# Optimization experiments

Measured on AMD Instinct MI355X. Metric: run time of the kernel, lower is better.

## Reference

```python
import math
import jax, jax.numpy as jnp
import numpy as np

CHANNELS = 512
OUT_CHANNELS = 512
N_HEADS = 8
K_CHANNELS = CHANNELS // N_HEADS
WINDOW = 4


def _get_relative_embeddings(emb, length):
    # emb: [1, 2*WINDOW+1, d] -> [1, 2*length-1, d]
    max_rel = 2 * WINDOW + 1
    pad_length = max(0, length - (WINDOW + 1))
    start = max(0, WINDOW + 1 - length)
    end = max_rel + 2 * length - 1
    if pad_length > 0:
        emb = jnp.pad(emb, ((0, 0), (pad_length, pad_length), (0, 0)))
    return emb[:, start:end]


def _rel_to_abs(x):
    # x: [b, h, l, 2l-1] -> [b, h, l, l] via skewing trick
    b, h, l, _ = x.shape
    x = jnp.pad(x, ((0, 0), (0, 0), (0, 0), (0, 1)))
    x_flat = x.reshape(b, h, l * 2 * l)
    x_flat = jnp.pad(x_flat, ((0, 0), (0, 0), (0, l - 1)))
    return x_flat.reshape(b, h, l + 1, 2 * l - 1)[..., :l, l - 1:]


def _abs_to_rel(x):
    # x: [b, h, l, l] -> [b, h, l, 2l-1]
    b, h, l, _ = x.shape
    x = jnp.pad(x, ((0, 0), (0, 0), (0, 0), (0, l - 1)))
    x_flat = x.reshape(b, h, -1)
    x_flat = jnp.pad(x_flat, ((0, 0), (0, 0), (l, 0)))
    return x_flat.reshape(b, h, l, 2 * l)[..., 1:]


def setup_inputs() -> dict:
    key = jax.random.key(0)
    ks = jax.random.split(key, 12)
    B, T = 4, 1024
    w_std = 1.0 / math.sqrt(CHANNELS)
    rel_std = K_CHANNELS ** (-0.5)
    return {
        'x': jax.random.normal(ks[0], (B, T, CHANNELS), jnp.float32),
        'c': jax.random.normal(ks[1], (B, T, CHANNELS), jnp.float32),
        'Wq': jax.random.normal(ks[2], (CHANNELS, CHANNELS), jnp.float32) * w_std,
        'bq': jnp.zeros((CHANNELS,), jnp.float32),
        'Wk': jax.random.normal(ks[3], (CHANNELS, CHANNELS), jnp.float32) * w_std,
        'bk': jnp.zeros((CHANNELS,), jnp.float32),
        'Wv': jax.random.normal(ks[4], (CHANNELS, CHANNELS), jnp.float32) * w_std,
        'bv': jnp.zeros((CHANNELS,), jnp.float32),
        'Wo': jax.random.normal(ks[5], (CHANNELS, OUT_CHANNELS), jnp.float32) * w_std,
        'bo': jnp.zeros((OUT_CHANNELS,), jnp.float32),
        'emb_rel_k': jax.random.normal(ks[6], (1, 2 * WINDOW + 1, K_CHANNELS), jnp.float32) * rel_std,
        'emb_rel_v': jax.random.normal(ks[7], (1, 2 * WINDOW + 1, K_CHANNELS), jnp.float32) * rel_std,
    }


def reference(x, c, Wq, bq, Wk, bk, Wv, bv, Wo, bo, emb_rel_k, emb_rel_v):
    b, t_t, _ = x.shape
    t_s = c.shape[1]
    # 1x1 convs == pointwise dense projections
    q = x @ Wq + bq
    k = c @ Wk + bk
    v = c @ Wv + bv
    q = q.reshape(b, t_t, N_HEADS, K_CHANNELS).transpose(0, 2, 1, 3)
    k = k.reshape(b, t_s, N_HEADS, K_CHANNELS).transpose(0, 2, 1, 3)
    v = v.reshape(b, t_s, N_HEADS, K_CHANNELS).transpose(0, 2, 1, 3)
    q_scaled = q / math.sqrt(K_CHANNELS)
    scores = jnp.einsum('bhtd,bhsd->bhts', q_scaled, k)
    # relative position bias via skewing trick (heads_share=True -> rel emb head dim 1)
    rel_k = _get_relative_embeddings(emb_rel_k, t_s)[0]  # [2*t_s-1, d]
    rel_logits = jnp.einsum('bhtd,md->bhtm', q_scaled, rel_k)
    scores = scores + _rel_to_abs(rel_logits)
    p_attn = jax.nn.softmax(scores, axis=-1)
    out = jnp.einsum('bhts,bhsd->bhtd', p_attn, v)
    rel_w = _abs_to_rel(p_attn)  # [b, h, t, 2t-1]
    rel_v = _get_relative_embeddings(emb_rel_v, t_s)[0]  # [2*t_s-1, d]
    out = out + jnp.einsum('bhtm,md->bhtd', rel_w, rel_v)
    out = out.transpose(0, 2, 1, 3).reshape(b, t_t, CHANNELS)
    return out @ Wo + bo
```

## Files before the change

kernel.cpp:

```cpp
#include <hip/hip_runtime.h>
#include <hip/hip_bf16.h>

#define B_ 4
#define T_ 1024
#define C_ 512
#define H_ 8

typedef __attribute__((ext_vector_type(8))) short short8;
typedef __attribute__((ext_vector_type(4))) float floatx4;

__device__ __forceinline__ unsigned short f2bs(float f) {
    __hip_bfloat16 h = __float2bfloat16(f);
    return *(unsigned short*)&h;
}
__device__ __forceinline__ float bs2f(unsigned short u) {
    __hip_bfloat16 h;
    *(unsigned short*)&h = u;
    return __bfloat162float(h);
}

__device__ __forceinline__ void gload_lds16(const void* g, void* l) {
    __builtin_amdgcn_global_load_lds(
        (const __attribute__((address_space(1))) unsigned int*)g,
        (__attribute__((address_space(3))) unsigned int*)l, 16, 0, 0);
}

__global__ __launch_bounds__(256) void prep(
    const float* __restrict__ Wq, const float* __restrict__ Wk,
    const float* __restrict__ Wv, const float* __restrict__ Wo,
    const float* __restrict__ x, const float* __restrict__ cc,
    unsigned short* __restrict__ WT,
    unsigned short* __restrict__ Xb, unsigned short* __restrict__ Cb)
{
    __shared__ unsigned short tileT[32][33];
    const int r = blockIdx.x, tid = threadIdx.x;
    if (r < 1024) {
        const int w = r >> 8, tile = r & 255;
        const int k0 = (tile >> 4) * 32, n0 = (tile & 15) * 32;
        const float* W = (w == 0) ? Wq : (w == 1) ? Wk : (w == 2) ? Wv : Wo;
        unsigned short* out = WT + (size_t)w * 512 * 512;
        const int kk = tid >> 3, ns = (tid & 7) * 4;
        const float4 v = *(const float4*)&W[(size_t)(k0 + kk) * 512 + n0 + ns];
        tileT[ns + 0][kk] = f2bs(v.x);
        tileT[ns + 1][kk] = f2bs(v.y);
        tileT[ns + 2][kk] = f2bs(v.z);
        tileT[ns + 3][kk] = f2bs(v.w);
        __syncthreads();
        const int nn = tid >> 3, ks = (tid & 7) * 4;
        ushort4 o;
        o.x = tileT[nn][ks + 0]; o.y = tileT[nn][ks + 1];
        o.z = tileT[nn][ks + 2]; o.w = tileT[nn][ks + 3];
        *(ushort4*)&out[(size_t)(n0 + nn) * 512 + k0 + ks] = o;
    } else {
        const int bi = r - 1024;
        const bool isx = bi < 1024;
        const float* src = isx ? x : cc;
        unsigned short* dst = isx ? Xb : Cb;
        const int gid = ((bi & 1023) * 256 + tid) * 8;
        const float4 v0 = *(const float4*)&src[gid];
        const float4 v1 = *(const float4*)&src[gid + 4];
        ushort4 a, b;
        a.x = f2bs(v0.x); a.y = f2bs(v0.y); a.z = f2bs(v0.z); a.w = f2bs(v0.w);
        b.x = f2bs(v1.x); b.y = f2bs(v1.y); b.z = f2bs(v1.z); b.w = f2bs(v1.w);
        *(ushort4*)&dst[gid] = a;
        *(ushort4*)&dst[gid + 4] = b;
    }
}

__global__ __launch_bounds__(256) void qkv_mfma(
    const unsigned short* __restrict__ Xb, const unsigned short* __restrict__ Cb,
    const unsigned short* __restrict__ WT,
    const float* __restrict__ bq, const float* __restrict__ bk,
    const float* __restrict__ bv,
    unsigned short* __restrict__ Qc, unsigned short* __restrict__ Kc,
    unsigned short* __restrict__ Vtg)
{
    const int z = blockIdx.z;
    const unsigned short* Ab = (z == 0) ? Xb : Cb;
    const unsigned short* Bt = WT + (size_t)z * 262144;
    const float* bias = (z == 0) ? bq : (z == 1) ? bk : bv;
    const float scale = (z == 0) ? 0.18033688011112042f  : 1.0f;

    __shared__ __align__(16) unsigned short sA[3 * 128 * 32];
    __shared__ __align__(16) unsigned short sB[3 * 128 * 32];

    const int tid = threadIdx.x;
    const int wave = tid >> 6, lane = tid & 63;
    const int m0 = blockIdx.y * 128, n0 = blockIdx.x * 128;
    const int mrow = lane & 15, quad = lane >> 4, kgrp = quad * 8;
    const int mhalf = (wave & 1) * 64, noff = (wave >> 1) * 64;
    const int lrow = lane >> 2, lseg = (lane & 3) * 16;

    floatx4 acc[4][4];
    #pragma unroll
    for (int i = 0; i < 4; i++)
        #pragma unroll
        for (int j = 0; j < 4; j++)
            acc[i][j] = (floatx4){0.f, 0.f, 0.f, 0.f};

    auto stage = [&](int k0, int bufi) {
        #pragma unroll
        for (int j = 0; j < 2; j++) {
            const int rr = wave * 32 + j * 16 + lrow;
            gload_lds16((const char*)Ab + ((size_t)(m0 + rr) * 512 + k0) * 2 + lseg,
                        &sA[(size_t)(bufi * 128 + wave * 32 + j * 16) * 32]);
            gload_lds16((const char*)Bt + ((size_t)(n0 + rr) * 512 + k0) * 2 + lseg,
                        &sB[(size_t)(bufi * 128 + wave * 32 + j * 16) * 32]);
        }
    };

    stage(0, 0);
    stage(32, 1);
    for (int ck = 0; ck < 16; ck++) {
        const int buf = ck % 3;
        if (ck < 15) asm volatile("s_waitcnt vmcnt(4)" ::: "memory");
        else         asm volatile("s_waitcnt vmcnt(0)" ::: "memory");
        __builtin_amdgcn_s_barrier();
        __builtin_amdgcn_sched_barrier(0);
        if (ck < 14) stage((ck + 2) * 32, (ck + 2) % 3);
        const unsigned short* sAb = sA + (size_t)buf * 128 * 32;
        const unsigned short* sBb = sB + (size_t)buf * 128 * 32;
        short8 af[4], bfv[4];
        #pragma unroll
        for (int i = 0; i < 4; i++)
            af[i] = *(const short8*)&sAb[(size_t)(mhalf + i * 16 + mrow) * 32 + kgrp];
        #pragma unroll
        for (int i = 0; i < 4; i++)
            bfv[i] = *(const short8*)&sBb[(size_t)(noff + i * 16 + mrow) * 32 + kgrp];
        #pragma unroll
        for (int mt = 0; mt < 4; mt++)
            #pragma unroll
            for (int nt = 0; nt < 4; nt++)
                acc[mt][nt] = __builtin_amdgcn_mfma_f32_16x16x32_bf16(
                    af[mt], bfv[nt], acc[mt][nt], 0, 0, 0);
    }

    const int rowq = quad * 4;
    if (z < 2) {
        unsigned short* Y = (z == 0) ? Qc : Kc;
        #pragma unroll
        for (int nt = 0; nt < 4; nt++) {
            const int n = n0 + noff + nt * 16 + mrow;
            const float bv_ = bias[n];
            const int h = n >> 6, d = n & 63;
            #pragma unroll
            for (int mt = 0; mt < 4; mt++)
                #pragma unroll
                for (int r = 0; r < 4; r++) {
                    const int m = m0 + mhalf + mt * 16 + rowq + r;
                    const int bb = m >> 10, t = m & 1023;
                    Y[(((size_t)bb * H_ + h) * 1024 + t) * 64 + d] =
                        f2bs((acc[mt][nt][r] + bv_) * scale);
                }
        }
    } else {
        #pragma unroll
        for (int nt = 0; nt < 4; nt++) {
            const int n = n0 + noff + nt * 16 + mrow;
            const float bv_ = bias[n];
            const int h = n >> 6, d = n & 63;
            #pragma unroll
            for (int mt = 0; mt < 4; mt++) {
                const int m = m0 + mhalf + mt * 16 + rowq;
                const int bb = m >> 10, t = m & 1023;
                ushort4 o4;
                o4.x = f2bs(acc[mt][nt][0] + bv_);
                o4.y = f2bs(acc[mt][nt][1] + bv_);
                o4.z = f2bs(acc[mt][nt][2] + bv_);
                o4.w = f2bs(acc[mt][nt][3] + bv_);
                *(ushort4*)&Vtg[(((size_t)bb * H_ + h) * 64 + d) * 1024 + t] = o4;
            }
        }
    }
}

__global__ __launch_bounds__(256) void out_mfma(
    const unsigned short* __restrict__ AOb, const unsigned short* __restrict__ WoT,
    const float* __restrict__ bias, float* __restrict__ out)
{
    __shared__ __align__(16) unsigned short sA[3 * 128 * 32];
    __shared__ __align__(16) unsigned short sB[3 * 64 * 32];

    const int tid = threadIdx.x;
    const int wave = tid >> 6, lane = tid & 63;
    const int m0 = blockIdx.y * 128, n0 = blockIdx.x * 64;
    const int mrow = lane & 15, quad = lane >> 4, kgrp = quad * 8;
    const int mhalf = (wave & 1) * 64, noff = (wave >> 1) * 32;
    const int lrow = lane >> 2, lseg = (lane & 3) * 16;

    floatx4 acc[4][2];
    #pragma unroll
    for (int i = 0; i < 4; i++)
        #pragma unroll
        for (int j = 0; j < 2; j++)
            acc[i][j] = (floatx4){0.f, 0.f, 0.f, 0.f};

    auto stage = [&](int k0, int bufi) {
        #pragma unroll
        for (int j = 0; j < 2; j++) {
            const int rA = wave * 32 + j * 16 + lrow;
            gload_lds16((const char*)AOb + ((size_t)(m0 + rA) * 512 + k0) * 2 + lseg,
                        &sA[(size_t)(bufi * 128 + wave * 32 + j * 16) * 32]);
        }
        const int rB = wave * 16 + lrow;
        gload_lds16((const char*)WoT + ((size_t)(n0 + rB) * 512 + k0) * 2 + lseg,
                    &sB[(size_t)(bufi * 64 + wave * 16) * 32]);
    };

    stage(0, 0);
    stage(32, 1);
    for (int ck = 0; ck < 16; ck++) {
        const int buf = ck % 3;
        if (ck < 15) asm volatile("s_waitcnt vmcnt(3)" ::: "memory");
        else         asm volatile("s_waitcnt vmcnt(0)" ::: "memory");
        __builtin_amdgcn_s_barrier();
        __builtin_amdgcn_sched_barrier(0);
        if (ck < 14) stage((ck + 2) * 32, (ck + 2) % 3);
        const unsigned short* sAb = sA + (size_t)buf * 128 * 32;
        const unsigned short* sBb = sB + (size_t)buf * 64 * 32;
        short8 af[4], bfv[2];
        #pragma unroll
        for (int i = 0; i < 4; i++)
            af[i] = *(const short8*)&sAb[(size_t)(mhalf + i * 16 + mrow) * 32 + kgrp];
        #pragma unroll
        for (int i = 0; i < 2; i++)
            bfv[i] = *(const short8*)&sBb[(size_t)(noff + i * 16 + mrow) * 32 + kgrp];
        #pragma unroll
        for (int mt = 0; mt < 4; mt++)
            #pragma unroll
            for (int nt = 0; nt < 2; nt++)
                acc[mt][nt] = __builtin_amdgcn_mfma_f32_16x16x32_bf16(
                    af[mt], bfv[nt], acc[mt][nt], 0, 0, 0);
    }

    const int rowq = quad * 4;
    #pragma unroll
    for (int nt = 0; nt < 2; nt++) {
        const int n = n0 + noff + nt * 16 + mrow;
        const float bv_ = bias[n];
        #pragma unroll
        for (int mt = 0; mt < 4; mt++)
            #pragma unroll
            for (int r = 0; r < 4; r++) {
                const int m = m0 + mhalf + mt * 16 + rowq + r;
                out[(size_t)m * 512 + n] = acc[mt][nt][r] + bv_;
            }
    }
}

__device__ __forceinline__ void attn_stage(
    const unsigned short* __restrict__ Kc, const unsigned short* __restrict__ Vtg,
    size_t qkbase, size_t vtbase, int s0, int wave, int ldrow, int gseg,
    unsigned short* KLb, unsigned short* VtLb)
{
    #pragma unroll
    for (int j = 0; j < 2; j++) {
        const int br = wave * 16 + j * 8;
        gload_lds16((const char*)Kc + (qkbase + (size_t)(s0 + br + ldrow) * 64) * 2 + gseg * 16,
                    &KLb[br * 64]);
        gload_lds16((const char*)Vtg + (vtbase + (size_t)(br + ldrow) * 1024 + s0) * 2 + gseg * 16,
                    &VtLb[br * 64]);
    }
}

__global__ __launch_bounds__(256) void attn_mfma(
    const unsigned short* __restrict__ Qc, const unsigned short* __restrict__ Kc,
    const unsigned short* __restrict__ Vtg,
    const float* __restrict__ rk, const float* __restrict__ rv,
    unsigned short* __restrict__ AOb)
{
    __shared__ __align__(16) unsigned short KL[3][64 * 64];
    __shared__ __align__(16) unsigned short VtL[3][64 * 64];
    __shared__ __align__(16) unsigned short PL[4][16 * 72];
    __shared__ float qbL[64 * 9];
    __shared__ float bandL[64 * 9];
    __shared__ float rvL[9 * 64];
    __shared__ float lL[64];

    const int tb = blockIdx.x, bh = blockIdx.y;
    const int b = bh >> 3, h = bh & 7;
    const int tid = threadIdx.x;
    const int wave = tid >> 6, lane = tid & 63;
    const int t0 = tb * 64;
    const int t0w = t0 + wave * 16;
    const size_t qkbase = (size_t)bh * T_ * 64;
    const size_t vtbase = (size_t)bh * 64 * T_;

    const int mrow = lane & 15;
    const int quad = lane >> 4;
    const int kgrp = quad * 8;
    const int x7 = mrow & 7;
    const int ldrow = lane >> 3;
    const int gseg = (lane & 7) ^ ldrow;

    attn_stage(Kc, Vtg, qkbase, vtbase, 0, wave, ldrow, gseg, &KL[0][0], &VtL[0][0]);
    attn_stage(Kc, Vtg, qkbase, vtbase, 64, wave, ldrow, gseg, &KL[1][0], &VtL[1][0]);

    for (int idx = tid; idx < 576; idx += 256) {
        bandL[idx] = 0.f;
        rvL[idx] = rv[idx];
        const int row = idx / 9, w = idx - row * 9;
        const unsigned short* qp = &Qc[qkbase + (size_t)(t0 + row) * 64];
        float s0a = 0.f, s1a = 0.f, s2a = 0.f, s3a = 0.f;
        #pragma unroll
        for (int d8 = 0; d8 < 8; d8 += 4) {
            const short8 q0 = *(const short8*)&qp[d8 * 8];
            const short8 q1 = *(const short8*)&qp[(d8 + 1) * 8];
            const short8 q2 = *(const short8*)&qp[(d8 + 2) * 8];
            const short8 q3 = *(const short8*)&qp[(d8 + 3) * 8];
            #pragma unroll
            for (int i = 0; i < 8; i++) {
                s0a = fmaf(bs2f((unsigned short)q0[i]), rk[w * 64 + d8 * 8 + i], s0a);
                s1a = fmaf(bs2f((unsigned short)q1[i]), rk[w * 64 + (d8 + 1) * 8 + i], s1a);
                s2a = fmaf(bs2f((unsigned short)q2[i]), rk[w * 64 + (d8 + 2) * 8 + i], s2a);
                s3a = fmaf(bs2f((unsigned short)q3[i]), rk[w * 64 + (d8 + 3) * 8 + i], s3a);
            }
        }
        qbL[idx] = (s0a + s1a) + (s2a + s3a);
    }

    const short8 aQ0 = *(const short8*)&Qc[qkbase + (size_t)(t0w + mrow) * 64 + kgrp];
    const short8 aQ1 = *(const short8*)&Qc[qkbase + (size_t)(t0w + mrow) * 64 + 32 + kgrp];

    floatx4 Oc[4];
    float lsA[4] = {0.f, 0.f, 0.f, 0.f};
    #pragma unroll
    for (int dt = 0; dt < 4; dt++) Oc[dt] = (floatx4){0.f, 0.f, 0.f, 0.f};

    unsigned short* Pw = &PL[wave][0];
    float* qbw = &qbL[wave * 16 * 9];
    float* bandw = &bandL[wave * 16 * 9];

    __syncthreads();

    for (int ck = 0; ck < 16; ck++) {
        const int s0 = ck * 64;
        const int buf = ck % 3;
        if (ck < 15) asm volatile("s_waitcnt vmcnt(4)" ::: "memory");
        else         asm volatile("s_waitcnt vmcnt(0)" ::: "memory");
        __builtin_amdgcn_s_barrier();
        __builtin_amdgcn_sched_barrier(0);
        if (ck < 14)
            attn_stage(Kc, Vtg, qkbase, vtbase, s0 + 128, wave, ldrow, gseg,
                       &KL[(ck + 2) % 3][0], &VtL[(ck + 2) % 3][0]);

        floatx4 Sc[4];
        #pragma unroll
        for (int st = 0; st < 4; st++) {
            const int row = st * 16 + mrow;
            const short8 aK0 = *(const short8*)&KL[buf][row * 64 + (quad ^ x7) * 8];
            const short8 aK1 = *(const short8*)&KL[buf][row * 64 + ((4 + quad) ^ x7) * 8];
            floatx4 s4 = {0.f, 0.f, 0.f, 0.f};
            s4 = __builtin_amdgcn_mfma_f32_16x16x32_bf16(aK0, aQ0, s4, 0, 0, 0);
            s4 = __builtin_amdgcn_mfma_f32_16x16x32_bf16(aK1, aQ1, s4, 0, 0, 0);
            Sc[st] = s4;
        }

        #pragma unroll
        for (int st = 0; st < 4; st++) {
            const int diff = s0 + st * 16 - t0w;
            float p0, p1, p2, p3;
            if (diff >= -19 && diff <= 19) {
                #pragma unroll
                for (int r = 0; r < 4; r++) {
                    const int rel = diff + quad * 4 + r - mrow;
                    float sc = Sc[st][r];
                    const bool inband = (rel >= -4) && (rel <= 4);
                    if (inband) sc += qbw[mrow * 9 + rel + 4];
                    const float p = __builtin_amdgcn_exp2f(sc);
                    if (inband) bandw[mrow * 9 + rel + 4] = p;
                    Sc[st][r] = p;
                }
            } else {
                #pragma unroll
                for (int r = 0; r < 4; r++)
                    Sc[st][r] = __builtin_amdgcn_exp2f(Sc[st][r]);
            }
            p0 = Sc[st][0]; p1 = Sc[st][1]; p2 = Sc[st][2]; p3 = Sc[st][3];
            lsA[st] += (p0 + p1) + (p2 + p3);
            ushort4 o4;
            o4.x = f2bs(p0); o4.y = f2bs(p1); o4.z = f2bs(p2); o4.w = f2bs(p3);
            *(ushort4*)&Pw[mrow * 72 + st * 16 + quad * 4] = o4;
        }

        #pragma unroll
        for (int c = 0; c < 2; c++) {
            const short8 aP = *(const short8*)&Pw[mrow * 72 + c * 32 + kgrp];
            #pragma unroll
            for (int dt = 0; dt < 4; dt++) {
                const int segl = (c * 4 + quad) ^ x7;
                const short8 bV = *(const short8*)&VtL[buf][(dt * 16 + mrow) * 64 + segl * 8];
                Oc[dt] = __builtin_amdgcn_mfma_f32_16x16x32_bf16(aP, bV, Oc[dt], 0, 0, 0);
            }
        }
    }

    float lv = (lsA[0] + lsA[1]) + (lsA[2] + lsA[3]);
    lv += __shfl_xor(lv, 16);
    lv += __shfl_xor(lv, 32);
    if (quad == 0) lL[wave * 16 + mrow] = lv;

    #pragma unroll
    for (int r = 0; r < 4; r++) {
        const int tl = quad * 4 + r;
        const float inv = 1.f / lL[wave * 16 + tl];
        #pragma unroll
        for (int w = 0; w < 9; w++) {
            const float p = bandw[tl * 9 + w];
            #pragma unroll
            for (int dt = 0; dt < 4; dt++)
                Oc[dt][r] = fmaf(p, rvL[w * 64 + dt * 16 + mrow], Oc[dt][r]);
        }
        const int t = t0w + tl;
        #pragma unroll
        for (int dt = 0; dt < 4; dt++)
            AOb[((size_t)b * 1024 + t) * 512 + h * 64 + dt * 16 + mrow] =
                f2bs(Oc[dt][r] * inv);
    }
}

extern "C" void kernel_launch(void* const* d_in, const int* in_sizes, int n_in,
                              void* d_out, int out_size, void* d_ws, size_t ws_size,
                              hipStream_t stream)
{
    const float* x  = (const float*)d_in[0];
    const float* c  = (const float*)d_in[1];
    const float* Wq = (const float*)d_in[2];
    const float* bq = (const float*)d_in[3];
    const float* Wk = (const float*)d_in[4];
    const float* bk = (const float*)d_in[5];
    const float* Wv = (const float*)d_in[6];
    const float* bv = (const float*)d_in[7];
    const float* Wo = (const float*)d_in[8];
    const float* bo = (const float*)d_in[9];
    const float* rk = (const float*)d_in[10];
    const float* rv = (const float*)d_in[11];

    unsigned short* WT  = (unsigned short*)d_ws;
    unsigned short* Qc  = WT + (size_t)4 * 512 * 512;
    unsigned short* Kc  = Qc + (size_t)32 * 1024 * 64;
    unsigned short* Vtg = Kc + (size_t)32 * 1024 * 64;
    unsigned short* AOb = Vtg + (size_t)32 * 1024 * 64;
    unsigned short* Xb  = AOb + (size_t)4096 * 512;
    unsigned short* Cb  = Xb + (size_t)4096 * 512;

    prep<<<3072, 256, 0, stream>>>(Wq, Wk, Wv, Wo, x, c, WT, Xb, Cb);
    qkv_mfma<<<dim3(4, 32, 3), 256, 0, stream>>>(Xb, Cb, WT, bq, bk, bv, Qc, Kc, Vtg);
    attn_mfma<<<dim3(16, 32), 256, 0, stream>>>(Qc, Kc, Vtg, rk, rv, AOb);
    out_mfma<<<dim3(8, 32), 256, 0, stream>>>(AOb, WT + (size_t)3 * 262144, bo, (float*)d_out);
}
```

Before: 150.5 us.

## Fuse all four stages into one cooperative persistent kernel with grid syncs

```diff
diff --git a/kernel.cpp b/kernel.cpp
--- a/kernel.cpp
+++ b/kernel.cpp
@@ -1,5 +1,8 @@
 #include <hip/hip_runtime.h>
 #include <hip/hip_bf16.h>
+#include <hip/hip_cooperative_groups.h>
+
+namespace cg = cooperative_groups;
 
 #define B_ 4
 #define T_ 1024
@@ -23,6 +26,399 @@
     __builtin_amdgcn_global_load_lds(
         (const __attribute__((address_space(1))) unsigned int*)g,
         (__attribute__((address_space(3))) unsigned int*)l, 16, 0, 0);
+}
+
+__device__ __forceinline__ void attn_stage(
+    const unsigned short* __restrict__ Kc, const unsigned short* __restrict__ Vtg,
+    size_t qkbase, size_t vtbase, int s0, int wave, int ldrow, int gseg,
+    unsigned short* KLb, unsigned short* VtLb)
+{
+    #pragma unroll
+    for (int j = 0; j < 2; j++) {
+        const int br = wave * 16 + j * 8;
+        gload_lds16((const char*)Kc + (qkbase + (size_t)(s0 + br + ldrow) * 64) * 2 + gseg * 16,
+                    &KLb[br * 64]);
+        gload_lds16((const char*)Vtg + (vtbase + (size_t)(br + ldrow) * 1024 + s0) * 2 + gseg * 16,
+                    &VtLb[br * 64]);
+    }
+}
+
+__global__ __launch_bounds__(256, 2) void fused(
+    const float* __restrict__ x, const float* __restrict__ cc,
+    const float* __restrict__ Wq, const float* __restrict__ bq,
+    const float* __restrict__ Wk, const float* __restrict__ bk,
+    const float* __restrict__ Wv, const float* __restrict__ bv,
+    const float* __restrict__ Wo, const float* __restrict__ bo,
+    const float* __restrict__ rk, const float* __restrict__ rv,
+    unsigned short* __restrict__ WT, unsigned short* __restrict__ Xb,
+    unsigned short* __restrict__ Cb, unsigned short* __restrict__ Qc,
+    unsigned short* __restrict__ Kc, unsigned short* __restrict__ Vtg,
+    unsigned short* __restrict__ AOb, float* __restrict__ out)
+{
+    __shared__ __align__(16) unsigned char smem[65536];
+    cg::grid_group grid = cg::this_grid();
+    const int bid = blockIdx.x;
+    const int tid = threadIdx.x;
+    const int wave = tid >> 6, lane = tid & 63;
+
+    {
+        unsigned short (*tileT)[33] = (unsigned short (*)[33])smem;
+        for (int u = bid; u < 3072; u += 512) {
+            __syncthreads();
+            if (u < 1024) {
+                const int w = u >> 8, tile = u & 255;
+                const int k0 = (tile >> 4) * 32, n0 = (tile & 15) * 32;
+                const float* W = (w == 0) ? Wq : (w == 1) ? Wk : (w == 2) ? Wv : Wo;
+                unsigned short* outp = WT + (size_t)w * 512 * 512;
+                const int kk = tid >> 3, ns = (tid & 7) * 4;
+                const float4 v = *(const float4*)&W[(size_t)(k0 + kk) * 512 + n0 + ns];
+                tileT[ns + 0][kk] = f2bs(v.x);
+                tileT[ns + 1][kk] = f2bs(v.y);
+                tileT[ns + 2][kk] = f2bs(v.z);
+                tileT[ns + 3][kk] = f2bs(v.w);
+                __syncthreads();
+                const int nn = tid >> 3, ks = (tid & 7) * 4;
+                ushort4 o;
+                o.x = tileT[nn][ks + 0]; o.y = tileT[nn][ks + 1];
+                o.z = tileT[nn][ks + 2]; o.w = tileT[nn][ks + 3];
+                *(ushort4*)&outp[(size_t)(n0 + nn) * 512 + k0 + ks] = o;
+            } else {
+                const int bi = u - 1024;
+                const bool isx = bi < 1024;
+                const float* src = isx ? x : cc;
+                unsigned short* dst = isx ? Xb : Cb;
+                const int gid = ((bi & 1023) * 256 + tid) * 8;
+                const float4 v0 = *(const float4*)&src[gid];
+                const float4 v1 = *(const float4*)&src[gid + 4];
+                ushort4 a, b;
+                a.x = f2bs(v0.x); a.y = f2bs(v0.y); a.z = f2bs(v0.z); a.w = f2bs(v0.w);
+                b.x = f2bs(v1.x); b.y = f2bs(v1.y); b.z = f2bs(v1.z); b.w = f2bs(v1.w);
+                *(ushort4*)&dst[gid] = a;
+                *(ushort4*)&dst[gid + 4] = b;
+            }
+        }
+    }
+    grid.sync();
+
+    if (bid < 384) {
+        const int z = bid >> 7, rem = bid & 127;
+        const int m0 = (rem >> 2) * 128, n0 = (rem & 3) * 128;
+        const unsigned short* Ab = (z == 0) ? Xb : Cb;
+        const unsigned short* Bt = WT + (size_t)z * 262144;
+        const float* bias = (z == 0) ? bq : (z == 1) ? bk : bv;
+        const float scale = (z == 0) ? 0.18033688011112042f  : 1.0f;
+
+        unsigned short* sA = (unsigned short*)smem;
+        unsigned short* sB = (unsigned short*)(smem + 24576);
+
+        const int mrow = lane & 15, quad = lane >> 4, kgrp = quad * 8;
+        const int mhalf = (wave & 1) * 64, noff = (wave >> 1) * 64;
+        const int lrow = lane >> 2, lseg = (lane & 3) * 16;
+
+        floatx4 acc[4][4];
+        #pragma unroll
+        for (int i = 0; i < 4; i++)
+            #pragma unroll
+            for (int j = 0; j < 4; j++)
+                acc[i][j] = (floatx4){0.f, 0.f, 0.f, 0.f};
+
+        auto stage = [&](int k0, int bufi) {
+            #pragma unroll
+            for (int j = 0; j < 2; j++) {
+                const int rr = wave * 32 + j * 16 + lrow;
+                gload_lds16((const char*)Ab + ((size_t)(m0 + rr) * 512 + k0) * 2 + lseg,
+                            &sA[(size_t)(bufi * 128 + wave * 32 + j * 16) * 32]);
+                gload_lds16((const char*)Bt + ((size_t)(n0 + rr) * 512 + k0) * 2 + lseg,
+                            &sB[(size_t)(bufi * 128 + wave * 32 + j * 16) * 32]);
+            }
+        };
+
+        stage(0, 0);
+        stage(32, 1);
+        for (int ck = 0; ck < 16; ck++) {
+            const int buf = ck % 3;
+            if (ck < 15) asm volatile("s_waitcnt vmcnt(4)" ::: "memory");
+            else         asm volatile("s_waitcnt vmcnt(0)" ::: "memory");
+            __builtin_amdgcn_s_barrier();
+            __builtin_amdgcn_sched_barrier(0);
+            if (ck < 14) stage((ck + 2) * 32, (ck + 2) % 3);
+            const unsigned short* sAb = sA + (size_t)buf * 128 * 32;
+            const unsigned short* sBb = sB + (size_t)buf * 128 * 32;
+            short8 af[4], bfv[4];
+            #pragma unroll
+            for (int i = 0; i < 4; i++)
+                af[i] = *(const short8*)&sAb[(size_t)(mhalf + i * 16 + mrow) * 32 + kgrp];
+            #pragma unroll
+            for (int i = 0; i < 4; i++)
+                bfv[i] = *(const short8*)&sBb[(size_t)(noff + i * 16 + mrow) * 32 + kgrp];
+            #pragma unroll
+            for (int mt = 0; mt < 4; mt++)
+                #pragma unroll
+                for (int nt = 0; nt < 4; nt++)
+                    acc[mt][nt] = __builtin_amdgcn_mfma_f32_16x16x32_bf16(
+                        af[mt], bfv[nt], acc[mt][nt], 0, 0, 0);
+        }
+
+        const int rowq = quad * 4;
+        if (z < 2) {
+            unsigned short* Y = (z == 0) ? Qc : Kc;
+            #pragma unroll
+            for (int nt = 0; nt < 4; nt++) {
+                const int n = n0 + noff + nt * 16 + mrow;
+                const float bv_ = bias[n];
+                const int h = n >> 6, d = n & 63;
+                #pragma unroll
+                for (int mt = 0; mt < 4; mt++)
+                    #pragma unroll
+                    for (int r = 0; r < 4; r++) {
+                        const int m = m0 + mhalf + mt * 16 + rowq + r;
+                        const int bb = m >> 10, t = m & 1023;
+                        Y[(((size_t)bb * H_ + h) * 1024 + t) * 64 + d] =
+                            f2bs((acc[mt][nt][r] + bv_) * scale);
+                    }
+            }
+        } else {
+            #pragma unroll
+            for (int nt = 0; nt < 4; nt++) {
+                const int n = n0 + noff + nt * 16 + mrow;
+                const float bv_ = bias[n];
+                const int h = n >> 6, d = n & 63;
+                #pragma unroll
+                for (int mt = 0; mt < 4; mt++) {
+                    const int m = m0 + mhalf + mt * 16 + rowq;
+                    const int bb = m >> 10, t = m & 1023;
+                    ushort4 o4;
+                    o4.x = f2bs(acc[mt][nt][0] + bv_);
+                    o4.y = f2bs(acc[mt][nt][1] + bv_);
+                    o4.z = f2bs(acc[mt][nt][2] + bv_);
+                    o4.w = f2bs(acc[mt][nt][3] + bv_);
+                    *(ushort4*)&Vtg[(((size_t)bb * H_ + h) * 64 + d) * 1024 + t] = o4;
+                }
+            }
+        }
+    }
+    grid.sync();
+
+    {
+        const int tb = bid & 15, bh = bid >> 4;
+        const int b = bh >> 3, h = bh & 7;
+        const int t0 = tb * 64;
+        const int t0w = t0 + wave * 16;
+        const size_t qkbase = (size_t)bh * T_ * 64;
+        const size_t vtbase = (size_t)bh * 64 * T_;
+
+        unsigned short* KL  = (unsigned short*)smem;
+        unsigned short* VtL = (unsigned short*)(smem + 24576);
+        unsigned short* PL  = (unsigned short*)(smem + 49152);
+        float* qbL   = (float*)(smem + 58368);
+        float* bandL = (float*)(smem + 60672);
+        float* rvL   = (float*)(smem + 62976);
+        float* lL    = (float*)(smem + 65280);
+
+        const int mrow = lane & 15;
+        const int quad = lane >> 4;
+        const int kgrp = quad * 8;
+        const int x7 = mrow & 7;
+        const int ldrow = lane >> 3;
+        const int gseg = (lane & 7) ^ ldrow;
+
+        attn_stage(Kc, Vtg, qkbase, vtbase, 0, wave, ldrow, gseg, KL, VtL);
+        attn_stage(Kc, Vtg, qkbase, vtbase, 64, wave, ldrow, gseg, KL + 4096, VtL + 4096);
+
+        for (int idx = tid; idx < 576; idx += 256) {
+            bandL[idx] = 0.f;
+            rvL[idx] = rv[idx];
+            const int row = idx / 9, w = idx - row * 9;
+            const unsigned short* qp = &Qc[qkbase + (size_t)(t0 + row) * 64];
+            float s0a = 0.f, s1a = 0.f, s2a = 0.f, s3a = 0.f;
+            #pragma unroll
+            for (int d8 = 0; d8 < 8; d8 += 4) {
+                const short8 q0 = *(const short8*)&qp[d8 * 8];
+                const short8 q1 = *(const short8*)&qp[(d8 + 1) * 8];
+                const short8 q2 = *(const short8*)&qp[(d8 + 2) * 8];
+                const short8 q3 = *(const short8*)&qp[(d8 + 3) * 8];
+                #pragma unroll
+                for (int i = 0; i < 8; i++) {
+                    s0a = fmaf(bs2f((unsigned short)q0[i]), rk[w * 64 + d8 * 8 + i], s0a);
+                    s1a = fmaf(bs2f((unsigned short)q1[i]), rk[w * 64 + (d8 + 1) * 8 + i], s1a);
+                    s2a = fmaf(bs2f((unsigned short)q2[i]), rk[w * 64 + (d8 + 2) * 8 + i], s2a);
+                    s3a = fmaf(bs2f((unsigned short)q3[i]), rk[w * 64 + (d8 + 3) * 8 + i], s3a);
+                }
+            }
+            qbL[idx] = (s0a + s1a) + (s2a + s3a);
+        }
+
+        const short8 aQ0 = *(const short8*)&Qc[qkbase + (size_t)(t0w + mrow) * 64 + kgrp];
+        const short8 aQ1 = *(const short8*)&Qc[qkbase + (size_t)(t0w + mrow) * 64 + 32 + kgrp];
+
+        floatx4 Oc[4];
+        float lsA[4] = {0.f, 0.f, 0.f, 0.f};
+        #pragma unroll
+        for (int dt = 0; dt < 4; dt++) Oc[dt] = (floatx4){0.f, 0.f, 0.f, 0.f};
+
+        unsigned short* Pw = PL + wave * 1152;
+        float* qbw = qbL + wave * 16 * 9;
+        float* bandw = bandL + wave * 16 * 9;
+
+        __syncthreads();
+
+        for (int ck = 0; ck < 16; ck++) {
+            const int s0 = ck * 64;
+            const int buf = ck % 3;
+            if (ck < 15) asm volatile("s_waitcnt vmcnt(4)" ::: "memory");
+            else         asm volatile("s_waitcnt vmcnt(0)" ::: "memory");
+            __builtin_amdgcn_s_barrier();
+            __builtin_amdgcn_sched_barrier(0);
+            if (ck < 14)
+                attn_stage(Kc, Vtg, qkbase, vtbase, s0 + 128, wave, ldrow, gseg,
+                           KL + ((ck + 2) % 3) * 4096, VtL + ((ck + 2) % 3) * 4096);
+
+            floatx4 Sc[4];
+            #pragma unroll
+            for (int st = 0; st < 4; st++) {
+                const int row = st * 16 + mrow;
+                const short8 aK0 = *(const short8*)&KL[buf * 4096 + row * 64 + (quad ^ x7) * 8];
+                const short8 aK1 = *(const short8*)&KL[buf * 4096 + row * 64 + ((4 + quad) ^ x7) * 8];
+                floatx4 s4 = {0.f, 0.f, 0.f, 0.f};
+                s4 = __builtin_amdgcn_mfma_f32_16x16x32_bf16(aK0, aQ0, s4, 0, 0, 0);
+                s4 = __builtin_amdgcn_mfma_f32_16x16x32_bf16(aK1, aQ1, s4, 0, 0, 0);
+                Sc[st] = s4;
+            }
+
+            #pragma unroll
+            for (int st = 0; st < 4; st++) {
+                const int diff = s0 + st * 16 - t0w;
+                float p0, p1, p2, p3;
+                if (diff >= -19 && diff <= 19) {
+                    #pragma unroll
+                    for (int r = 0; r < 4; r++) {
+                        const int rel = diff + quad * 4 + r - mrow;
+                        float sc = Sc[st][r];
+                        const bool inband = (rel >= -4) && (rel <= 4);
+                        if (inband) sc += qbw[mrow * 9 + rel + 4];
+                        const float p = __builtin_amdgcn_exp2f(sc);
+                        if (inband) bandw[mrow * 9 + rel + 4] = p;
+                        Sc[st][r] = p;
+                    }
+                } else {
+                    #pragma unroll
+                    for (int r = 0; r < 4; r++)
+                        Sc[st][r] = __builtin_amdgcn_exp2f(Sc[st][r]);
+                }
+                p0 = Sc[st][0]; p1 = Sc[st][1]; p2 = Sc[st][2]; p3 = Sc[st][3];
+                lsA[st] += (p0 + p1) + (p2 + p3);
+                ushort4 o4;
+                o4.x = f2bs(p0); o4.y = f2bs(p1); o4.z = f2bs(p2); o4.w = f2bs(p3);
+                *(ushort4*)&Pw[mrow * 72 + st * 16 + quad * 4] = o4;
+            }
+
+            #pragma unroll
+            for (int c = 0; c < 2; c++) {
+                const short8 aP = *(const short8*)&Pw[mrow * 72 + c * 32 + kgrp];
+                #pragma unroll
+                for (int dt = 0; dt < 4; dt++) {
+                    const int segl = (c * 4 + quad) ^ x7;
+                    const short8 bV = *(const short8*)&VtL[buf * 4096 + (dt * 16 + mrow) * 64 + segl * 8];
+                    Oc[dt] = __builtin_amdgcn_mfma_f32_16x16x32_bf16(aP, bV, Oc[dt], 0, 0, 0);
+                }
+            }
+        }
+
+        float lv = (lsA[0] + lsA[1]) + (lsA[2] + lsA[3]);
+        lv += __shfl_xor(lv, 16);
+        lv += __shfl_xor(lv, 32);
+        if (quad == 0) lL[wave * 16 + mrow] = lv;
+
+        #pragma unroll
+        for (int r = 0; r < 4; r++) {
+            const int tl = quad * 4 + r;
+            const float inv = 1.f / lL[wave * 16 + tl];
+            #pragma unroll
+            for (int w = 0; w < 9; w++) {
+                const float p = bandw[tl * 9 + w];
+                #pragma unroll
+                for (int dt = 0; dt < 4; dt++)
+                    Oc[dt][r] = fmaf(p, rvL[w * 64 + dt * 16 + mrow], Oc[dt][r]);
+            }
+            const int t = t0w + tl;
+            #pragma unroll
+            for (int dt = 0; dt < 4; dt++)
+                AOb[((size_t)b * 1024 + t) * 512 + h * 64 + dt * 16 + mrow] =
+                    f2bs(Oc[dt][r] * inv);
+        }
+    }
+    grid.sync();
+
+    if (bid < 256) {
+        const int m0 = (bid >> 3) * 128, n0 = (bid & 7) * 64;
+        const unsigned short* WoT = WT + (size_t)3 * 262144;
+
+        unsigned short* sA = (unsigned short*)smem;
+        unsigned short* sB = (unsigned short*)(smem + 24576);
+
+        const int mrow = lane & 15, quad = lane >> 4, kgrp = quad * 8;
+        const int mhalf = (wave & 1) * 64, noff = (wave >> 1) * 32;
+        const int lrow = lane >> 2, lseg = (lane & 3) * 16;
+
+        floatx4 acc[4][2];
+        #pragma unroll
+        for (int i = 0; i < 4; i++)
+            #pragma unroll
+            for (int j = 0; j < 2; j++)
+                acc[i][j] = (floatx4){0.f, 0.f, 0.f, 0.f};
+
+        auto stage = [&](int k0, int bufi) {
+            #pragma unroll
+            for (int j = 0; j < 2; j++) {
+                const int rA = wave * 32 + j * 16 + lrow;
+                gload_lds16((const char*)AOb + ((size_t)(m0 + rA) * 512 + k0) * 2 + lseg,
+                            &sA[(size_t)(bufi * 128 + wave * 32 + j * 16) * 32]);
+            }
+            const int rB = wave * 16 + lrow;
+            gload_lds16((const char*)WoT + ((size_t)(n0 + rB) * 512 + k0) * 2 + lseg,
+                        &sB[(size_t)(bufi * 64 + wave * 16) * 32]);
+        };
+
+        stage(0, 0);
+        stage(32, 1);
+        for (int ck = 0; ck < 16; ck++) {
+            const int buf = ck % 3;
+            if (ck < 15) asm volatile("s_waitcnt vmcnt(3)" ::: "memory");
+            else         asm volatile("s_waitcnt vmcnt(0)" ::: "memory");
+            __builtin_amdgcn_s_barrier();
+            __builtin_amdgcn_sched_barrier(0);
+            if (ck < 14) stage((ck + 2) * 32, (ck + 2) % 3);
+            const unsigned short* sAb = sA + (size_t)buf * 128 * 32;
+            const unsigned short* sBb = sB + (size_t)buf * 64 * 32;
+            short8 af[4], bfv[2];
+            #pragma unroll
+            for (int i = 0; i < 4; i++)
+                af[i] = *(const short8*)&sAb[(size_t)(mhalf + i * 16 + mrow) * 32 + kgrp];
+            #pragma unroll
+            for (int i = 0; i < 2; i++)
+                bfv[i] = *(const short8*)&sBb[(size_t)(noff + i * 16 + mrow) * 32 + kgrp];
+            #pragma unroll
+            for (int mt = 0; mt < 4; mt++)
+                #pragma unroll
+                for (int nt = 0; nt < 2; nt++)
+                    acc[mt][nt] = __builtin_amdgcn_mfma_f32_16x16x32_bf16(
+                        af[mt], bfv[nt], acc[mt][nt], 0, 0, 0);
+        }
+
+        const int rowq = quad * 4;
+        #pragma unroll
+        for (int nt = 0; nt < 2; nt++) {
+            const int n = n0 + noff + nt * 16 + mrow;
+            const float bv_ = bo[n];
+            #pragma unroll
+            for (int mt = 0; mt < 4; mt++)
+                #pragma unroll
+                for (int r = 0; r < 4; r++) {
+                    const int m = m0 + mhalf + mt * 16 + rowq + r;
+                    out[(size_t)m * 512 + n] = acc[mt][nt][r] + bv_;
+                }
+        }
+    }
 }
 
 __global__ __launch_bounds__(256) void prep(
@@ -79,7 +475,7 @@
     const unsigned short* Ab = (z == 0) ? Xb : Cb;
     const unsigned short* Bt = WT + (size_t)z * 262144;
     const float* bias = (z == 0) ? bq : (z == 1) ? bk : bv;
-    const float scale = (z == 0) ? 0.18033688011112042f  : 1.0f;
+    const float scale = (z == 0) ? 0.18033688011112042f : 1.0f;
 
     __shared__ __align__(16) unsigned short sA[3 * 128 * 32];
     __shared__ __align__(16) unsigned short sB[3 * 128 * 32];
@@ -245,21 +641,6 @@
                 const int m = m0 + mhalf + mt * 16 + rowq + r;
                 out[(size_t)m * 512 + n] = acc[mt][nt][r] + bv_;
             }
-    }
-}
-
-__device__ __forceinline__ void attn_stage(
-    const unsigned short* __restrict__ Kc, const unsigned short* __restrict__ Vtg,
-    size_t qkbase, size_t vtbase, int s0, int wave, int ldrow, int gseg,
-    unsigned short* KLb, unsigned short* VtLb)
-{
-    #pragma unroll
-    for (int j = 0; j < 2; j++) {
-        const int br = wave * 16 + j * 8;
-        gload_lds16((const char*)Kc + (qkbase + (size_t)(s0 + br + ldrow) * 64) * 2 + gseg * 16,
-                    &KLb[br * 64]);
-        gload_lds16((const char*)Vtg + (vtbase + (size_t)(br + ldrow) * 1024 + s0) * 2 + gseg * 16,
-                    &VtLb[br * 64]);
     }
 }
 
@@ -443,9 +824,32 @@
     unsigned short* AOb = Vtg + (size_t)32 * 1024 * 64;
     unsigned short* Xb  = AOb + (size_t)4096 * 512;
     unsigned short* Cb  = Xb + (size_t)4096 * 512;
-
-    prep<<<3072, 256, 0, stream>>>(Wq, Wk, Wv, Wo, x, c, WT, Xb, Cb);
-    qkv_mfma<<<dim3(4, 32, 3), 256, 0, stream>>>(Xb, Cb, WT, bq, bk, bv, Qc, Kc, Vtg);
-    attn_mfma<<<dim3(16, 32), 256, 0, stream>>>(Qc, Kc, Vtg, rk, rv, AOb);
-    out_mfma<<<dim3(8, 32), 256, 0, stream>>>(AOb, WT + (size_t)3 * 262144, bo, (float*)d_out);
-}
+    float* outp = (float*)d_out;
+
+    static int coop = -1;
+    if (coop < 0) {
+        int v = 0;
+        hipDeviceGetAttribute(&v, hipDeviceAttributeCooperativeLaunch, 0);
+        coop = v;
+    }
+
+    bool launched = false;
+    if (coop) {
+        void* params[20] = {
+            (void*)&x, (void*)&c, (void*)&Wq, (void*)&bq, (void*)&Wk, (void*)&bk,
+            (void*)&Wv, (void*)&bv, (void*)&Wo, (void*)&bo, (void*)&rk, (void*)&rv,
+            (void*)&WT, (void*)&Xb, (void*)&Cb, (void*)&Qc, (void*)&Kc, (void*)&Vtg,
+            (void*)&AOb, (void*)&outp };
+        hipError_t e = hipLaunchCooperativeKernel((const void*)fused, dim3(512),
+                                                  dim3(256), params, 0, stream);
+        if (e == hipSuccess) launched = true;
+        else (void)hipGetLastError();
+    }
+
+    if (!launched) {
+        prep<<<3072, 256, 0, stream>>>(Wq, Wk, Wv, Wo, x, c, WT, Xb, Cb);
+        qkv_mfma<<<dim3(4, 32, 3), 256, 0, stream>>>(Xb, Cb, WT, bq, bk, bv, Qc, Kc, Vtg);
+        attn_mfma<<<dim3(16, 32), 256, 0, stream>>>(Qc, Kc, Vtg, rk, rv, AOb);
+        out_mfma<<<dim3(8, 32), 256, 0, stream>>>(AOb, WT + (size_t)3 * 262144, bo, outp);
+    }
+}
```

Result: slower. 345.0 us (+129.3%).
